# Performance work log

Hardware: AMD Instinct MI355X
Metric: run time of the kernel (lower is better)

The kernel has to match this reference:

```python
import jax, jax.numpy as jnp
from jax import lax
import numpy as np

KERNEL_SIZE = 15
CHANNELS = 3
PAD = KERNEL_SIZE // 2


def _make_kernels(sigma):
    """Gaussian kernels [B, K, K], normalized to sum 1 (matches torch create_kernel)."""
    k = KERNEL_SIZE
    ax = jnp.linspace(-(k - 1) / 2.0, (k - 1) / 2.0, k, dtype=sigma.dtype)
    xx, yy = jnp.meshgrid(ax, ax, indexing='ij')  # [K, K]
    s = sigma.reshape(-1, 1, 1)  # [B, 1, 1]
    kern = jnp.exp(-(xx[None] ** 2 + yy[None] ** 2) / (2.0 * s ** 2 + 1e-8))
    kern = kern / (kern.sum(axis=(-1, -2), keepdims=True) + 1e-8)
    return kern  # [B, K, K]


def setup_inputs() -> dict:
    key = jax.random.key(0)
    k1, k2 = jax.random.split(key)
    x = jax.random.normal(k1, (32, CHANNELS, 512, 512), dtype=jnp.float32)
    # sigma in (0.5, 3.0): realistic blur stddevs, strictly positive
    sigma = jax.random.uniform(k2, (32,), dtype=jnp.float32, minval=0.5, maxval=3.0)
    return {"x": x, "sigma": sigma}


def reference(x, sigma):
    B, C, H, W = x.shape
    kern = _make_kernels(sigma)  # [B, K, K]

    def conv_one(xi, ki):
        # xi: [C, H, W], ki: [K, K]; same kernel replicated per channel (depthwise)
        w = jnp.broadcast_to(ki[None, None], (C, 1, KERNEL_SIZE, KERNEL_SIZE))
        out = lax.conv_general_dilated(
            xi[None],  # [1, C, H, W]
            w,         # [C, 1, K, K]
            window_strides=(1, 1),
            padding=[(PAD, PAD), (PAD, PAD)],
            feature_group_count=C,
        )
        return out[0]  # [C, H, W]

    return jax.vmap(conv_one)(x, kern)  # [B, C, H, W]
```

## Files before the change

### kernel.cpp

```cpp
#include <hip/hip_runtime.h>

#define CHANNELS 3
#define HW 512
#define KS 15
#define GPAD 7
#define TILE 64
#define HT (TILE + 2 * GPAD)
#define IN_STR 81
#define WCOLS 20
#define WIN (16 + KS - 1)

__global__ __launch_bounds__(256, 6)
void gauss_blur_kernel(const float* __restrict__ x,
                       const float* __restrict__ sigma,
                       float* __restrict__ out) {
    __shared__ float in_s[HT * IN_STR];

    const int tid   = threadIdx.x;
    const int tileX = blockIdx.x;
    const int tileY = blockIdx.y;
    const int bc    = blockIdx.z;
    const int b     = bc / CHANNELS;

    float w[KS];
    {
        const float s = sigma[b];
        const float inv_denom = 1.0f / (2.0f * s * s + 1e-8f);
        float sum = 0.0f;
        #pragma unroll
        for (int i = 0; i < KS; ++i) {
            const float d = (float)(i - GPAD);
            const float g = __expf(-d * d * inv_denom);
            w[i] = g;
            sum += g;
        }
        const float inv = 1.0f / sum;
        #pragma unroll
        for (int i = 0; i < KS; ++i) w[i] *= inv;
    }

    const size_t plane = (size_t)HW * HW;
    const float* xp = x + (size_t)bc * plane;
    float* op       = out + (size_t)bc * plane;
    const int gx0 = tileX * TILE;
    const int gy0 = tileY * TILE - GPAD;
    const int ax0 = gx0 - 8;

    for (int i = tid; i < HT * WCOLS; i += 256) {
        const int r = i / WCOLS;
        const int q = i - r * WCOLS;
        const int gy = gy0 + r;
        const int gc = ax0 + 4 * q;
        float4 v = make_float4(0.f, 0.f, 0.f, 0.f);
        if ((unsigned)gy < (unsigned)HW) {
            const float* rowp = xp + (size_t)gy * HW;
            if (gc >= 0 && gc + 4 <= HW) {
                v = *(const float4*)(rowp + gc);
            } else {
                if ((unsigned)(gc + 0) < (unsigned)HW) v.x = rowp[gc + 0];
                if ((unsigned)(gc + 1) < (unsigned)HW) v.y = rowp[gc + 1];
                if ((unsigned)(gc + 2) < (unsigned)HW) v.z = rowp[gc + 2];
                if ((unsigned)(gc + 3) < (unsigned)HW) v.w = rowp[gc + 3];
            }
        }
        float* d = &in_s[r * IN_STR + 4 * q];
        d[0] = v.x; d[1] = v.y; d[2] = v.z; d[3] = v.w;
    }
    __syncthreads();

    float acc[2][16];
    #pragma unroll
    for (int p = 0; p < 2; ++p)
        #pragma unroll
        for (int o = 0; o < 16; ++o) acc[p][o] = 0.0f;

    #pragma unroll
    for (int p = 0; p < 2; ++p) {
        const int i = tid + p * 256;
        if (i < HT * 4) {
            const int r  = i >> 2;
            const int ch = i & 3;
            const float* src = &in_s[r * IN_STR + 16 * ch + 1];
            #pragma unroll
            for (int j = 0; j < WIN; ++j) {
                const float v = src[j];
                const int lo = (j - (KS - 1)) > 0 ? (j - (KS - 1)) : 0;
                const int hi = (j < 15) ? j : 15;
                #pragma unroll
                for (int o = lo; o <= hi; ++o)
                    acc[p][o] = fmaf(w[j - o], v, acc[p][o]);
            }
        }
    }
    __syncthreads();

    #pragma unroll
    for (int p = 0; p < 2; ++p) {
        const int i = tid + p * 256;
        if (i < HT * 4) {
            const int r  = i >> 2;
            const int ch = i & 3;
            float* dst = &in_s[r * IN_STR + 16 * ch];
            #pragma unroll
            for (int o = 0; o < 16; ++o) dst[o] = acc[p][o];
        }
    }
    __syncthreads();

    {
        const int c  = tid & (TILE - 1);
        const int r0 = (tid >> 6) * 16;
        float vacc[16];
        #pragma unroll
        for (int o = 0; o < 16; ++o) vacc[o] = 0.0f;
        #pragma unroll
        for (int j = 0; j < WIN; ++j) {
            const float v = in_s[(r0 + j) * IN_STR + c];
            const int lo = (j - (KS - 1)) > 0 ? (j - (KS - 1)) : 0;
            const int hi = (j < 15) ? j : 15;
            #pragma unroll
            for (int o = lo; o <= hi; ++o) vacc[o] = fmaf(w[j - o], v, vacc[o]);
        }
        const int gx = gx0 + c;
        #pragma unroll
        for (int o = 0; o < 16; ++o)
            op[(size_t)(tileY * TILE + r0 + o) * HW + gx] = vacc[o];
    }
}

extern "C" void kernel_launch(void* const* d_in, const int* in_sizes, int n_in,
                              void* d_out, int out_size, void* d_ws, size_t ws_size,
                              hipStream_t stream) {
    const float* x     = (const float*)d_in[0];
    const float* sigma = (const float*)d_in[1];
    float* out         = (float*)d_out;
    const int B = in_sizes[1];
    dim3 grid(HW / TILE, HW / TILE, B * CHANNELS);
    gauss_blur_kernel<<<grid, dim3(256, 1, 1), 0, stream>>>(x, sigma, out);
}
```

Measured before the change: 191.9 us.

## Load horizontal windows directly from global into registers, dropping input smem stage

The horizontal pass now reads each thread's 32-wide row window straight from global memory into registers, using float4 loads for interior tiles. This removes the raw-input shared-memory staging buffer and one barrier, and shrinks LDS to a single 78x65 intermediate so the launch bound can target 8 blocks. Gaussian weights are forced into scalar registers with readfirstlane. Neighbouring threads now overlap in their global reads (32 floats read for 16 outputs), and register pressure from the window array may fight the higher occupancy target.

New measurement: 245.5 us. +28.0%, slower.

```diff
diff --git a/kernel.cpp b/kernel.cpp
--- a/kernel.cpp
+++ b/kernel.cpp
@@ -6,15 +6,14 @@
 #define GPAD 7
 #define TILE 64
 #define HT (TILE + 2 * GPAD)
-#define IN_STR 81
-#define WCOLS 20
+#define MSTR 65
 #define WIN (16 + KS - 1)
 
-__global__ __launch_bounds__(256, 6)
+__global__ __launch_bounds__(256, 8)
 void gauss_blur_kernel(const float* __restrict__ x,
                        const float* __restrict__ sigma,
                        float* __restrict__ out) {
-    __shared__ float in_s[HT * IN_STR];
+    __shared__ float mid_s[HT * MSTR];
 
     const int tid   = threadIdx.x;
     const int tileX = blockIdx.x;
@@ -26,17 +25,18 @@
     {
         const float s = sigma[b];
         const float inv_denom = 1.0f / (2.0f * s * s + 1e-8f);
+        float g[KS];
         float sum = 0.0f;
         #pragma unroll
         for (int i = 0; i < KS; ++i) {
             const float d = (float)(i - GPAD);
-            const float g = __expf(-d * d * inv_denom);
-            w[i] = g;
-            sum += g;
+            g[i] = __expf(-d * d * inv_denom);
+            sum += g[i];
         }
         const float inv = 1.0f / sum;
         #pragma unroll
-        for (int i = 0; i < KS; ++i) w[i] *= inv;
+        for (int i = 0; i < KS; ++i)
+            w[i] = __int_as_float(__builtin_amdgcn_readfirstlane(__float_as_int(g[i] * inv)));
     }
 
     const size_t plane = (size_t)HW * HW;
@@ -44,65 +44,47 @@
     float* op       = out + (size_t)bc * plane;
     const int gx0 = tileX * TILE;
     const int gy0 = tileY * TILE - GPAD;
-    const int ax0 = gx0 - 8;
+    const bool xin = (tileX > 0) && (tileX < (HW / TILE) - 1);
 
-    for (int i = tid; i < HT * WCOLS; i += 256) {
-        const int r = i / WCOLS;
-        const int q = i - r * WCOLS;
+    for (int i = tid; i < HT * 4; i += 256) {
+        const int r  = i >> 2;
+        const int ch = i & 3;
         const int gy = gy0 + r;
-        const int gc = ax0 + 4 * q;
-        float4 v = make_float4(0.f, 0.f, 0.f, 0.f);
-        if ((unsigned)gy < (unsigned)HW) {
-            const float* rowp = xp + (size_t)gy * HW;
-            if (gc >= 0 && gc + 4 <= HW) {
-                v = *(const float4*)(rowp + gc);
-            } else {
-                if ((unsigned)(gc + 0) < (unsigned)HW) v.x = rowp[gc + 0];
-                if ((unsigned)(gc + 1) < (unsigned)HW) v.y = rowp[gc + 1];
-                if ((unsigned)(gc + 2) < (unsigned)HW) v.z = rowp[gc + 2];
-                if ((unsigned)(gc + 3) < (unsigned)HW) v.w = rowp[gc + 3];
+        float* dst = &mid_s[r * MSTR + 16 * ch];
+        if ((unsigned)gy >= (unsigned)HW) {
+            #pragma unroll
+            for (int o = 0; o < 16; ++o) dst[o] = 0.0f;
+            continue;
+        }
+        const int c0 = gx0 + 16 * ch - 8;
+        const float* rowp = xp + (size_t)gy * HW + c0;
+        float win[32];
+        if (xin) {
+            #pragma unroll
+            for (int k = 0; k < 8; ++k) {
+                const float4 v = *(const float4*)(rowp + 4 * k);
+                win[4 * k + 0] = v.x; win[4 * k + 1] = v.y;
+                win[4 * k + 2] = v.z; win[4 * k + 3] = v.w;
+            }
+        } else {
+            #pragma unroll
+            for (int k = 0; k < 32; ++k) {
+                const int gc = c0 + k;
+                win[k] = ((unsigned)gc < (unsigned)HW) ? rowp[k] : 0.0f;
             }
         }
-        float* d = &in_s[r * IN_STR + 4 * q];
-        d[0] = v.x; d[1] = v.y; d[2] = v.z; d[3] = v.w;
-    }
-    __syncthreads();
-
-    float acc[2][16];
-    #pragma unroll
-    for (int p = 0; p < 2; ++p)
+        float acc[16];
         #pragma unroll
-        for (int o = 0; o < 16; ++o) acc[p][o] = 0.0f;
-
-    #pragma unroll
-    for (int p = 0; p < 2; ++p) {
-        const int i = tid + p * 256;
-        if (i < HT * 4) {
-            const int r  = i >> 2;
-            const int ch = i & 3;
-            const float* src = &in_s[r * IN_STR + 16 * ch + 1];
+        for (int o = 0; o < 16; ++o) acc[o] = 0.0f;
+        #pragma unroll
+        for (int j = 0; j < WIN; ++j) {
+            const float v = win[j + 1];
+            const int lo = (j - (KS - 1)) > 0 ? (j - (KS - 1)) : 0;
+            const int hi = (j < 15) ? j : 15;
             #pragma unroll
-            for (int j = 0; j < WIN; ++j) {
-                const float v = src[j];
-                const int lo = (j - (KS - 1)) > 0 ? (j - (KS - 1)) : 0;
-                const int hi = (j < 15) ? j : 15;
-                #pragma unroll
-                for (int o = lo; o <= hi; ++o)
-                    acc[p][o] = fmaf(w[j - o], v, acc[p][o]);
-            }
-        }
-    }
-    __syncthreads();
-
-    #pragma unroll
-    for (int p = 0; p < 2; ++p) {
-        const int i = tid + p * 256;
-        if (i < HT * 4) {
-            const int r  = i >> 2;
-            const int ch = i & 3;
-            float* dst = &in_s[r * IN_STR + 16 * ch];
-            #pragma unroll
-            for (int o = 0; o < 16; ++o) dst[o] = acc[p][o];
+            for (int o = lo; o <= hi; ++o)
+                acc[o] = fmaf(w[j - o], v, acc[o]);
+            if (j >= KS - 1) dst[j - (KS - 1)] = acc[j - (KS - 1)];
         }
     }
     __syncthreads();
@@ -115,16 +97,17 @@
         for (int o = 0; o < 16; ++o) vacc[o] = 0.0f;
         #pragma unroll
         for (int j = 0; j < WIN; ++j) {
-            const float v = in_s[(r0 + j) * IN_STR + c];
+            const float v = mid_s[(r0 + j) * MSTR + c];
             const int lo = (j - (KS - 1)) > 0 ? (j - (KS - 1)) : 0;
             const int hi = (j < 15) ? j : 15;
             #pragma unroll
             for (int o = lo; o <= hi; ++o) vacc[o] = fmaf(w[j - o], v, vacc[o]);
         }
         const int gx = gx0 + c;
+        float* colp = op + (size_t)(tileY * TILE + r0) * HW + gx;
         #pragma unroll
         for (int o = 0; o < 16; ++o)
-            op[(size_t)(tileY * TILE + r0 + o) * HW + gx] = vacc[o];
+            colp[(size_t)o * HW] = vacc[o];
     }
 }
 
```
